# Kernel optimization log

Measured on AMD Instinct MI355X. Metric: run time of the kernel, lower is better.

## Reference

```python
import jax, jax.numpy as jnp
import numpy as np

EMBED_DIM = 768
NUM_HEADS = 12
HEAD_DIM = EMBED_DIM // NUM_HEADS // 2  # 32
MLP_DIM = 3072
DEPTH = 1
LAMBDA_INIT = 0.8 - 0.6 * float(np.exp(-0.3 * (DEPTH - 1)))  # 0.2
EPS = 1e-5


def layernorm(x, g, b):
    mu = jnp.mean(x, axis=-1, keepdims=True)
    var = jnp.mean((x - mu) ** 2, axis=-1, keepdims=True)
    return (x - mu) * jax.lax.rsqrt(var + EPS) * g + b


def rmsnorm(x, g):
    ms = jnp.mean(x ** 2, axis=-1, keepdims=True)
    return x * jax.lax.rsqrt(ms + EPS) * g


def setup_inputs() -> dict:
    key = jax.random.key(0)
    ks = jax.random.split(key, 16)
    d, m, hd = EMBED_DIM, MLP_DIM, HEAD_DIM
    inp = {
        "x": jax.random.normal(ks[0], (32, 577, d), dtype=jnp.float32),
        "ln1_g": jnp.ones((d,), jnp.float32),
        "ln1_b": jnp.zeros((d,), jnp.float32),
        "wq": jax.random.normal(ks[1], (d, d), jnp.float32) * 0.02,
        "wk": jax.random.normal(ks[2], (d, d), jnp.float32) * 0.02,
        "wv": jax.random.normal(ks[3], (d, d), jnp.float32) * 0.02,
        "wo": jax.random.normal(ks[4], (d, d), jnp.float32) * 0.02,
        "lq1": jax.random.normal(ks[5], (hd,), jnp.float32) * 0.1,
        "lk1": jax.random.normal(ks[6], (hd,), jnp.float32) * 0.1,
        "lq2": jax.random.normal(ks[7], (hd,), jnp.float32) * 0.1,
        "lk2": jax.random.normal(ks[8], (hd,), jnp.float32) * 0.1,
        "subln_g": jnp.ones((2 * hd,), jnp.float32),
        "ln2_g": jnp.ones((d,), jnp.float32),
        "ln2_b": jnp.zeros((d,), jnp.float32),
        "w1": jax.random.normal(ks[9], (m, d), jnp.float32) * 0.02,
        "b1": jnp.zeros((m,), jnp.float32),
        "w2": jax.random.normal(ks[10], (d, m), jnp.float32) * 0.02,
        "b2": jnp.zeros((d,), jnp.float32),
    }
    return inp


def diff_attn(x, wq, wk, wv, wo, lq1, lk1, lq2, lk2, subln_g):
    b, n, d = x.shape
    h, hd = NUM_HEADS, HEAD_DIM
    q = (x @ wq.T).reshape(b, n, 2 * h, hd)  # [b,n,2h,hd]
    k = (x @ wk.T).reshape(b, n, 2 * h, hd)
    v = (x @ wv.T).reshape(b, n, h, 2 * hd)  # [b,n,h,2hd]
    scale = hd ** -0.5
    scores = jnp.einsum("bnhd,bmhd->bhnm", q * scale, k)  # [b,2h,n,n]
    probs = jax.nn.softmax(scores.astype(jnp.float32), axis=-1).astype(x.dtype)
    probs = probs.reshape(b, h, 2, n, n)
    lam = jnp.exp(jnp.sum(lq1 * lk1)) - jnp.exp(jnp.sum(lq2 * lk2)) + LAMBDA_INIT
    attn = probs[:, :, 0] - lam * probs[:, :, 1]  # [b,h,n,n]
    out = jnp.einsum("bhnm,bmhe->bnhe", attn, v)  # [b,n,h,2hd]
    out = rmsnorm(out, subln_g) * (1.0 - LAMBDA_INIT)
    return out.reshape(b, n, d) @ wo.T


def reference(x, ln1_g, ln1_b, wq, wk, wv, wo, lq1, lk1, lq2, lk2, subln_g,
              ln2_g, ln2_b, w1, b1, w2, b2):
    # pre-LN -> differential attention -> residual
    a = diff_attn(layernorm(x, ln1_g, ln1_b), wq, wk, wv, wo,
                  lq1, lk1, lq2, lk2, subln_g)
    x = x + a
    # pre-LN -> GELU MLP -> residual (dropout = 0 / eval)
    h = layernorm(x, ln2_g, ln2_b)
    h = jax.nn.gelu(h @ w1.T + b1, approximate=False) @ w2.T + b2
    return x + h
```

## Files before the change

### kernel.cpp

```cpp
#include <hip/hip_runtime.h>
#include <hip/hip_bf16.h>
#include <cstdint>
#include <cstddef>

typedef __bf16 bf16_t;
typedef __attribute__((ext_vector_type(8))) __bf16 bf16x8;
typedef __attribute__((ext_vector_type(4))) __bf16 bf16x4;
typedef __attribute__((ext_vector_type(4))) float f32x4;
typedef __attribute__((ext_vector_type(4))) int int4v;
typedef __attribute__((ext_vector_type(2))) unsigned uintx2;

#define DEV static __device__ __forceinline__

#define BATCH 32
#define SEQ 577
#define DMODEL 768
#define MROWS (BATCH * SEQ)
#define MPAD 18688
#define NH 12
#define HDIM 32
#define EDIM 64
#define MLPD 3072
#define NPAD 640
#define QKVSTR 2304

DEV f32x4 mfma16(bf16x8 a, bf16x8 b, f32x4 c) {
    return __builtin_amdgcn_mfma_f32_16x16x32_bf16(a, b, c, 0, 0, 0);
}

DEV void gload16(const void* g, void* l) {
    __builtin_amdgcn_global_load_lds(
        (const __attribute__((address_space(1))) void*)(uintptr_t)g,
        (__attribute__((address_space(3))) void*)(uintptr_t)l,
        16, 0, 0);
}

DEV unsigned cvt_pk_bf16(float lo, float hi) {
    unsigned r;
    asm("v_cvt_pk_bf16_f32 %0, %1, %2" : "=v"(r) : "v"(lo), "v"(hi));
    return r;
}
DEV void plane16_swap(unsigned& a, unsigned& b) {
    asm("v_permlane16_swap_b32 %0, %1" : "+v"(a), "+v"(b));
}
DEV void plane32_swap(unsigned& a, unsigned& b) {
    asm("v_permlane32_swap_b32 %0, %1" : "+v"(a), "+v"(b));
}

DEV int xcd_swz(int orig, int nwg) {
    const int q = nwg >> 3, r = nwg & 7;
    const int xcd = orig & 7, loc = orig >> 3;
    return (xcd < r ? xcd * (q + 1) : r * (q + 1) + (xcd - r) * q) + loc;
}

__global__ __launch_bounds__(256)
void wconv_kernel(const float* __restrict__ wq, const float* __restrict__ wk,
                  const float* __restrict__ wv, const float* __restrict__ wo,
                  const float* __restrict__ w1, const float* __restrict__ w2,
                  bf16_t* __restrict__ dst)
{
    const size_t idx = ((size_t)blockIdx.x * 256 + threadIdx.x) * 4;
    const float* src;
    size_t off;
    if      (idx <  589824) { src = wq; off = idx; }
    else if (idx < 1179648) { src = wk; off = idx - 589824; }
    else if (idx < 1769472) { src = wv; off = idx - 1179648; }
    else if (idx < 2359296) { src = wo; off = idx - 1769472; }
    else if (idx < 4718592) { src = w1; off = idx - 2359296; }
    else                    { src = w2; off = idx - 4718592; }
    const f32x4 v = *(const f32x4*)&src[off];
    bf16x4 o;
#pragma unroll
    for (int u = 0; u < 4; ++u) o[u] = (bf16_t)v[u];
    *(bf16x4*)&dst[idx] = o;
}

__global__ void lam_kernel(const float* __restrict__ lq1, const float* __restrict__ lk1,
                           const float* __restrict__ lq2, const float* __restrict__ lk2,
                           float* __restrict__ lam)
{
    const int l = threadIdx.x;
    float a = 0.f, c = 0.f;
    if (l < 32) { a = lq1[l] * lk1[l]; c = lq2[l] * lk2[l]; }
#pragma unroll
    for (int m = 1; m < 32; m <<= 1) { a += __shfl_xor(a, m); c += __shfl_xor(c, m); }
    if (l == 0) *lam = expf(a) - expf(c) + 0.2f;
}

__global__ __launch_bounds__(256)
void ln_kernel(const float* __restrict__ src, const float* __restrict__ g,
               const float* __restrict__ bt, bf16_t* __restrict__ dst, const int Mv)
{
    const int row = blockIdx.x;
    const int t = threadIdx.x;
    if (row >= Mv) {
        for (int i = t; i < DMODEL; i += 256) dst[(size_t)row * DMODEL + i] = (bf16_t)0.f;
        return;
    }
    const float* p = src + (size_t)row * DMODEL;
    const float v0 = p[t], v1 = p[t + 256], v2 = p[t + 512];
    float s = v0 + v1 + v2, s2 = v0 * v0 + v1 * v1 + v2 * v2;
#pragma unroll
    for (int m = 1; m < 64; m <<= 1) { s += __shfl_xor(s, m); s2 += __shfl_xor(s2, m); }
    __shared__ float red[8];
    const int w = t >> 6;
    if ((t & 63) == 0) { red[w] = s; red[4 + w] = s2; }
    __syncthreads();
    s  = red[0] + red[1] + red[2] + red[3];
    s2 = red[4] + red[5] + red[6] + red[7];
    const float mu  = s * (1.f / DMODEL);
    const float var = s2 * (1.f / DMODEL) - mu * mu;
    const float rs = rsqrtf(var + 1e-5f);
    bf16_t* d = dst + (size_t)row * DMODEL;
    d[t      ] = (bf16_t)((v0 - mu) * rs * g[t      ] + bt[t      ]);
    d[t + 256] = (bf16_t)((v1 - mu) * rs * g[t + 256] + bt[t + 256]);
    d[t + 512] = (bf16_t)((v2 - mu) * rs * g[t + 512] + bt[t + 512]);
}

#define VM3 asm volatile("s_waitcnt vmcnt(3)" ::: "memory")
#define VM0 asm volatile("s_waitcnt vmcnt(0)" ::: "memory")
#define SB0 __builtin_amdgcn_sched_barrier(0)
#define BAR __builtin_amdgcn_s_barrier()

#define ASZ 4096
#define BSZ 8192

#define QUAD8(H, BP)                                                         \
    do {                                                                     \
        __builtin_amdgcn_s_setprio(1);                                       \
        _Pragma("unroll")                                                    \
        for (int m2_ = 0; m2_ < 4; ++m2_)                                    \
            _Pragma("unroll")                                                \
            for (int j_ = 0; j_ < 2; ++j_)                                   \
                acc[m2_][(H) * 2 + j_] =                                     \
                    mfma16(af[m2_], BP[j_], acc[m2_][(H) * 2 + j_]);         \
        __builtin_amdgcn_s_setprio(0);                                       \
    } while (0)

template <int EPI>
__global__ __launch_bounds__(512, 4)
void gemm4(const bf16_t* __restrict__ A, const bf16_t* __restrict__ W,
           const int K, const int N, const int NT,
           bf16_t* __restrict__ outB, float* __restrict__ outF,
           const float* __restrict__ bias, const float* __restrict__ resid,
           const int Mv)
{
    __shared__ bf16_t As[3 * ASZ];
    __shared__ bf16_t Bs[3 * BSZ];
    const int t = threadIdx.x;
    const int l = t & 63, w = t >> 6;
    const int lg = l >> 4, lc = l & 15;
    const int wr = w >> 2, wc = w & 3;

    const int nwg = gridDim.x * gridDim.y;
    const int orig = blockIdx.y * gridDim.x + blockIdx.x;
    const int wg = xcd_swz(orig, nwg);
    const int tileRow = (wg / gridDim.y) * 128;
    const int tileCol = (wg % gridDim.y) * 256;

    const int srow = t >> 2;
    const int csrc = ((t & 3) ^ ((t >> 3) & 3)) * 8;
    const bf16_t* srcA  = A + (size_t)(tileRow + srow) * K + csrc;
    const bf16_t* srcB0 = W + (size_t)(tileCol + srow) * K + csrc;
    const bf16_t* srcB1 = W + (size_t)(tileCol + 128 + srow) * K + csrc;

    f32x4 acc[4][4];
#pragma unroll
    for (int m = 0; m < 4; ++m)
#pragma unroll
        for (int n = 0; n < 4; ++n) acc[m][n] = f32x4{0.f, 0.f, 0.f, 0.f};

    const int rch = (lg ^ ((lc >> 1) & 3)) * 8;
    const int aoff = (wr * 64 + lc) * 32 + rch;
    const int boff = (wc * 64 + lc) * 32 + rch;

    bf16x8 af[4], b01[2], b23[2];

    auto stageA = [&](int kt, bf16_t* dst) {
        gload16(srcA + (size_t)kt * 32, dst + t * 8);
    };
    auto stageB = [&](int kt, bf16_t* dst) {
        gload16(srcB0 + (size_t)kt * 32, dst + t * 8);
        gload16(srcB1 + (size_t)kt * 32, dst + (t + 512) * 8);
    };
    auto rdA = [&](const bf16_t* buf) {
#pragma unroll
        for (int m2 = 0; m2 < 4; ++m2)
            af[m2] = *(const bf16x8*)&buf[aoff + m2 * 512];
    };
    auto rdB = [&](const bf16_t* buf, int h, bf16x8* bp) {
#pragma unroll
        for (int j = 0; j < 2; ++j)
            bp[j] = *(const bf16x8*)&buf[boff + (h * 2 + j) * 512];
    };

    auto STEP = [&](int kt, const bf16_t* AsR, const bf16_t* BsR,
                    bf16_t* AsS, bf16_t* BsS) {
        rdA(AsR); rdB(BsR, 0, b01);
        if (kt + 2 < NT) stageA(kt + 2, AsS);
        SB0; BAR; SB0;
        QUAD8(0, b01);
        BAR;
        rdB(BsR, 1, b23);
        if (kt + 2 < NT) stageB(kt + 2, BsS);
        if (kt == NT - 2) { VM0; } else if (kt < NT - 2) { VM3; }
        SB0; BAR; SB0;
        QUAD8(1, b23);
        BAR;
    };

    stageA(0, As);          stageB(0, Bs);
    stageA(1, As + ASZ);    stageB(1, Bs + BSZ);
    VM3; BAR;

#pragma unroll 1
    for (int kt = 0; kt < NT; kt += 3) {
        STEP(kt,     As,           Bs,           As + 2 * ASZ, Bs + 2 * BSZ);
        STEP(kt + 1, As + ASZ,     Bs + BSZ,     As,           Bs);
        STEP(kt + 2, As + 2 * ASZ, Bs + 2 * BSZ, As + ASZ,     Bs + BSZ);
    }

#pragma unroll
    for (int m = 0; m < 4; ++m) {
        const int row0 = tileRow + wr * 64 + m * 16 + 4 * lg;
#pragma unroll
        for (int n = 0; n < 4; ++n) {
            const int col = tileCol + wc * 64 + n * 16 + lc;
#pragma unroll
            for (int r = 0; r < 4; ++r) {
                const int row = row0 + r;
                float v = acc[m][n][r];
                if (EPI == 0) {
                    outB[(size_t)row * N + col] = (bf16_t)v;
                } else if (EPI == 1) {
                    const float xin = (row < Mv) ? resid[(size_t)row * N + col] : 0.f;
                    outF[(size_t)row * N + col] = v + xin;
                } else if (EPI == 2) {
                    v += bias[col];
                    v = 0.5f * v * (1.f + erff(v * 0.70710678118654752f));
                    outB[(size_t)row * N + col] = (bf16_t)v;
                } else {
                    if (row < Mv)
                        outF[(size_t)row * N + col] = v + bias[col] + resid[(size_t)row * N + col];
                }
            }
        }
    }
}

__global__ __launch_bounds__(256)
void vtrans_kernel(const bf16_t* __restrict__ qkv, bf16_t* __restrict__ vt)
{
    const int nt = blockIdx.x, h = blockIdx.y, b = blockIdx.z;
    const int t = threadIdx.x;
    __shared__ bf16_t T[64][72];
    {
        const int nl = t >> 2, e0 = (t & 3) * 16;
        const int n = nt * 64 + nl;
        bf16x8 a, c;
        if (n < SEQ) {
            const bf16_t* src = &qkv[((size_t)b * SEQ + n) * QKVSTR + 1536 + h * EDIM + e0];
            a = *(const bf16x8*)src;
            c = *(const bf16x8*)(src + 8);
        } else {
#pragma unroll
            for (int u = 0; u < 8; ++u) { a[u] = (bf16_t)0.f; c[u] = (bf16_t)0.f; }
        }
#pragma unroll
        for (int u = 0; u < 8; ++u) { T[e0 + u][nl] = a[u]; T[e0 + 8 + u][nl] = c[u]; }
    }
    __syncthreads();
    {
        const int e = t >> 2, n0 = (t & 3) * 16;
        bf16x8 a, c;
#pragma unroll
        for (int u = 0; u < 8; ++u) { a[u] = T[e][n0 + u]; c[u] = T[e][n0 + 8 + u]; }
        bf16_t* d = &vt[((size_t)(b * NH + h) * EDIM + e) * NPAD + nt * 64 + n0];
        *(bf16x8*)d = a;
        *(bf16x8*)(d + 8) = c;
    }
}

__global__ __launch_bounds__(256)
void attn_kernel(const bf16_t* __restrict__ qkv, const bf16_t* __restrict__ vtp,
                 const float* __restrict__ lamp, const float* __restrict__ subg,
                 bf16_t* __restrict__ outp)
{
    const int orig = blockIdx.x + 10 * (blockIdx.y + 12 * blockIdx.z);
    const int wg = xcd_swz(orig, 3840);
    const int qt = wg % 10;
    const int h  = (wg / 10) % 12;
    const int b  = wg / 120;
    const int t = threadIdx.x, w = t >> 6, l = t & 63;
    const int lg = l >> 4, lc = l & 15;
    const float lam = *lamp;
    const float SC2 = 0.25503487f;
    const float MARG = 8.0f * 0.25503487f;

    __shared__ bf16_t Ks[2][64 * 64];
    __shared__ bf16_t Vs[2][64 * 64];

    const size_t mb = (size_t)b * SEQ;
    const int q0row = qt * 64 + w * 16;

    bf16x8 qf[2];
#pragma unroll
    for (int hh = 0; hh < 2; ++hh)
        qf[hh] = *(const bf16x8*)&qkv[(mb + q0row + lc) * QKVSTR
                                      + h * 64 + hh * 32 + 8 * lg];

    f32x4 O[2][4];
    f32x4 Ol[2];
#pragma unroll
    for (int hh = 0; hh < 2; ++hh) {
        Ol[hh] = f32x4{0.f, 0.f, 0.f, 0.f};
#pragma unroll
        for (int ef = 0; ef < 4; ++ef) O[hh][ef] = f32x4{0.f, 0.f, 0.f, 0.f};
    }

    bf16x8 ones;
#pragma unroll
    for (int u = 0; u < 8; ++u) ones[u] = (bf16_t)1.0f;

    const int r0 = t >> 3, c0 = (t & 7);
    const int r1 = r0 + 32;
    const bf16_t* kg0 = &qkv[(mb + r0) * QKVSTR + 768 + h * 64 + ((c0 ^ (r0 & 7)) * 8)];
    const bf16_t* kg1 = &qkv[(mb + r1) * QKVSTR + 768 + h * 64 + ((c0 ^ (r1 & 7)) * 8)];
    const bf16_t* vg0 = &vtp[(size_t)((b * NH + h) * EDIM + r0) * NPAD + ((c0 ^ (r0 & 7)) * 8)];
    const bf16_t* vg1 = &vtp[(size_t)((b * NH + h) * EDIM + r1) * NPAD + ((c0 ^ (r1 & 7)) * 8)];

    auto stage = [&](int kt, int bufi) {
        gload16(kg0 + (size_t)kt * (64 * QKVSTR), &Ks[bufi][t * 8]);
        gload16(kg1 + (size_t)kt * (64 * QKVSTR), &Ks[bufi][(t + 256) * 8]);
        gload16(vg0 + kt * 64, &Vs[bufi][t * 8]);
        gload16(vg1 + kt * 64, &Vs[bufi][(t + 256) * 8]);
    };

    stage(0, 0);
    int buf = 0;

    const int swz = lc & 7;
    int koff[2], voff[2];
#pragma unroll
    for (int hh = 0; hh < 2; ++hh) koff[hh] = lc * 64 + (((hh * 4 + lg) ^ swz) * 8);
#pragma unroll
    for (int ks = 0; ks < 2; ++ks) voff[ks] = lc * 64 + (((ks * 4 + lg) ^ swz) * 8);

#pragma unroll 1
    for (int kt = 0; kt < 10; ++kt) {
        __builtin_amdgcn_s_barrier();
        if (kt < 9) {
            stage(kt + 1, buf ^ 1);
            asm volatile("s_waitcnt vmcnt(4)" ::: "memory");
        } else {
            VM0;
        }
        __builtin_amdgcn_s_barrier();
        __builtin_amdgcn_sched_barrier(0);

        const bf16_t* Kb = &Ks[buf][0];
        const bf16_t* Vb = &Vs[buf][0];

#pragma unroll
        for (int hh = 0; hh < 2; ++hh) {
            bf16x8 kf[4];
#pragma unroll
            for (int f = 0; f < 4; ++f)
                kf[f] = *(const bf16x8*)&Kb[koff[hh] + f * 1024];
            f32x4 s[4];
#pragma unroll
            for (int f = 0; f < 4; ++f)
                s[f] = mfma16(kf[f], qf[hh], f32x4{0.f, 0.f, 0.f, 0.f});
            if (kt == 9) {
#pragma unroll
                for (int f = 0; f < 4; ++f)
#pragma unroll
                    for (int r = 0; r < 4; ++r)
                        if (f | r) s[f][r] = -3e38f;
                if (lg != 0) s[0][0] = -3e38f;
            }
            unsigned wd[4][2];
#pragma unroll
            for (int f = 0; f < 4; ++f) {
                float p0 = __builtin_amdgcn_exp2f(__builtin_fmaf(s[f][0], SC2, -MARG));
                float p1 = __builtin_amdgcn_exp2f(__builtin_fmaf(s[f][1], SC2, -MARG));
                float p2 = __builtin_amdgcn_exp2f(__builtin_fmaf(s[f][2], SC2, -MARG));
                float p3 = __builtin_amdgcn_exp2f(__builtin_fmaf(s[f][3], SC2, -MARG));
                wd[f][0] = cvt_pk_bf16(p0, p1);
                wd[f][1] = cvt_pk_bf16(p2, p3);
            }
#pragma unroll
            for (int half = 0; half < 2; ++half) {
#pragma unroll
                for (int p = 0; p < 2; ++p) {
                    unsigned& Aa = wd[half * 2][p];
                    unsigned& Bb = wd[half * 2 + 1][p];
                    plane32_swap(Aa, Bb);
                    plane16_swap(Aa, Bb);
                }
            }
            const bf16x8 pa0 = __builtin_bit_cast(bf16x8,
                int4v{(int)wd[0][0], (int)wd[0][1], (int)wd[1][0], (int)wd[1][1]});
            const bf16x8 pa1 = __builtin_bit_cast(bf16x8,
                int4v{(int)wd[2][0], (int)wd[2][1], (int)wd[3][0], (int)wd[3][1]});

#pragma unroll
            for (int ef = 0; ef < 4; ++ef) {
                const bf16x8 vb0 = *(const bf16x8*)&Vb[voff[0] + ef * 1024];
                const bf16x8 vb1 = *(const bf16x8*)&Vb[voff[1] + ef * 1024];
                O[hh][ef] = mfma16(vb0, pa0, O[hh][ef]);
                O[hh][ef] = mfma16(vb1, pa1, O[hh][ef]);
            }
            Ol[hh] = mfma16(ones, pa0, Ol[hh]);
            Ol[hh] = mfma16(ones, pa1, Ol[hh]);
        }
        buf ^= 1;
    }

    {
        const float i0 = 1.f / Ol[0][0];
        const float i1 = lam / Ol[1][0];
        float comb[4][4];
        float ms = 0.f;
#pragma unroll
        for (int ef = 0; ef < 4; ++ef)
#pragma unroll
            for (int r = 0; r < 4; ++r) {
                const float o = O[0][ef][r] * i0 - O[1][ef][r] * i1;
                comb[ef][r] = o;
                ms += o * o;
            }
        ms += __shfl_xor(ms, 16);
        ms += __shfl_xor(ms, 32);
        const float sc = rsqrtf(ms * (1.f / 64.f) + 1e-5f) * 0.8f;
        const int nq = q0row + lc;
        if (nq < SEQ) {
            bf16_t* dst = &outp[(mb + nq) * DMODEL + h * EDIM + 4 * lg];
#pragma unroll
            for (int ef = 0; ef < 4; ++ef) {
                const f32x4 g4 = *(const f32x4*)&subg[ef * 16 + 4 * lg];
                const unsigned u0 = cvt_pk_bf16(comb[ef][0] * sc * g4[0],
                                                comb[ef][1] * sc * g4[1]);
                const unsigned u1 = cvt_pk_bf16(comb[ef][2] * sc * g4[2],
                                                comb[ef][3] * sc * g4[3]);
                *(uintx2*)(dst + ef * 16) = uintx2{u0, u1};
            }
        }
    }
}

extern "C" void kernel_launch(void* const* d_in, const int* in_sizes, int n_in,
                              void* d_out, int out_size, void* d_ws, size_t ws_size,
                              hipStream_t stream)
{
    const float* x    = (const float*)d_in[0];
    const float* ln1g = (const float*)d_in[1];
    const float* ln1b = (const float*)d_in[2];
    const float* wq   = (const float*)d_in[3];
    const float* wk   = (const float*)d_in[4];
    const float* wv   = (const float*)d_in[5];
    const float* wo   = (const float*)d_in[6];
    const float* lq1  = (const float*)d_in[7];
    const float* lk1  = (const float*)d_in[8];
    const float* lq2  = (const float*)d_in[9];
    const float* lk2  = (const float*)d_in[10];
    const float* subg = (const float*)d_in[11];
    const float* ln2g = (const float*)d_in[12];
    const float* ln2b = (const float*)d_in[13];
    const float* w1   = (const float*)d_in[14];
    const float* b1   = (const float*)d_in[15];
    const float* w2   = (const float*)d_in[16];
    const float* b2   = (const float*)d_in[17];

    char* ws = (char*)d_ws;
    bf16_t* wAll = (bf16_t*)ws;
    bf16_t* wob = wAll + 1769472;
    bf16_t* w1b = wAll + 2359296;
    bf16_t* w2b = wAll + 4718592;
    ws += 7077888ull * 2;
    float* lamP = (float*)ws; ws += 256;
    bf16_t* xn   = (bf16_t*)ws; ws += (size_t)MPAD * DMODEL * 2;
    bf16_t* qkvb = (bf16_t*)ws;
    bf16_t* h1   = qkvb;
    ws += (size_t)MPAD * QKVSTR * 2;
    bf16_t* vtb  = (bf16_t*)ws; ws += (size_t)(BATCH * NH) * EDIM * NPAD * 2;
    bf16_t* aout = (bf16_t*)ws; ws += (size_t)MPAD * DMODEL * 2;
    float* x1    = (float*)ws;  ws += (size_t)MPAD * DMODEL * 4;

    wconv_kernel<<<6912, 256, 0, stream>>>(wq, wk, wv, wo, w1, w2, wAll);
    lam_kernel<<<1, 64, 0, stream>>>(lq1, lk1, lq2, lk2, lamP);
    ln_kernel<<<MPAD, 256, 0, stream>>>(x, ln1g, ln1b, xn, MROWS);

    gemm4<0><<<dim3(146, 9), 512, 0, stream>>>(xn, wAll, 768, QKVSTR, 24,
                                               qkvb, nullptr, nullptr, nullptr, MROWS);

    vtrans_kernel<<<dim3(10, 12, 32), 256, 0, stream>>>(qkvb, vtb);
    attn_kernel<<<dim3(10, 12, 32), 256, 0, stream>>>(qkvb, vtb, lamP, subg, aout);

    gemm4<1><<<dim3(146, 3), 512, 0, stream>>>(aout, wob, 768, 768, 24,
                                               nullptr, x1, nullptr, x, MROWS);
    ln_kernel<<<MPAD, 256, 0, stream>>>(x1, ln2g, ln2b, xn, MROWS);
    gemm4<2><<<dim3(146, 12), 512, 0, stream>>>(xn, w1b, 768, MLPD, 24,
                                                h1, nullptr, b1, nullptr, MROWS);
    gemm4<3><<<dim3(146, 3), 512, 0, stream>>>(h1, w2b, MLPD, 768, 96,
                                               nullptr, (float*)d_out, b2, x1, MROWS);
}
```

Before: 559.1 us.

## Split attention differential halves across separate waves with 512-thread blocks

The attention kernel now launches 512 threads. Each pair of waves handles one 16-row query slice, with one wave per differential half (hh), instead of a single wave looping over both halves. The second-half wave writes its O accumulators and row sums to shared memory reused from the K/V buffers, and the first-half wave combines them after a barrier. This doubles the waves available to hide latency and halves per-wave register pressure, at the cost of an extra LDS round trip and barrier in the epilogue.

```diff
diff --git a/kernel.cpp b/kernel.cpp
--- a/kernel.cpp
+++ b/kernel.cpp
@@ -118,6 +118,7 @@
 }
 
 #define VM3 asm volatile("s_waitcnt vmcnt(3)" ::: "memory")
+#define VM2 asm volatile("s_waitcnt vmcnt(2)" ::: "memory")
 #define VM0 asm volatile("s_waitcnt vmcnt(0)" ::: "memory")
 #define SB0 __builtin_amdgcn_sched_barrier(0)
 #define BAR __builtin_amdgcn_s_barrier()
@@ -281,7 +282,7 @@
     }
 }
 
-__global__ __launch_bounds__(256)
+__global__ __launch_bounds__(512)
 void attn_kernel(const bf16_t* __restrict__ qkv, const bf16_t* __restrict__ vtp,
                  const float* __restrict__ lamp, const float* __restrict__ subg,
                  bf16_t* __restrict__ outp)
@@ -293,6 +294,7 @@
     const int b  = wg / 120;
     const int t = threadIdx.x, w = t >> 6, l = t & 63;
     const int lg = l >> 4, lc = l & 15;
+    const int qsub = w >> 1, hh = w & 1;
     const float lam = *lamp;
     const float SC2 = 0.25503487f;
     const float MARG = 8.0f * 0.25503487f;
@@ -301,132 +303,133 @@
     __shared__ bf16_t Vs[2][64 * 64];
 
     const size_t mb = (size_t)b * SEQ;
-    const int q0row = qt * 64 + w * 16;
-
-    bf16x8 qf[2];
-#pragma unroll
-    for (int hh = 0; hh < 2; ++hh)
-        qf[hh] = *(const bf16x8*)&qkv[(mb + q0row + lc) * QKVSTR
-                                      + h * 64 + hh * 32 + 8 * lg];
-
-    f32x4 O[2][4];
-    f32x4 Ol[2];
-#pragma unroll
-    for (int hh = 0; hh < 2; ++hh) {
-        Ol[hh] = f32x4{0.f, 0.f, 0.f, 0.f};
-#pragma unroll
-        for (int ef = 0; ef < 4; ++ef) O[hh][ef] = f32x4{0.f, 0.f, 0.f, 0.f};
-    }
+    const int q0row = qt * 64 + qsub * 16;
+
+    const bf16x8 qf = *(const bf16x8*)&qkv[(mb + q0row + lc) * QKVSTR
+                                           + h * 64 + hh * 32 + 8 * lg];
+
+    f32x4 O[4];
+    f32x4 Ol = f32x4{0.f, 0.f, 0.f, 0.f};
+#pragma unroll
+    for (int ef = 0; ef < 4; ++ef) O[ef] = f32x4{0.f, 0.f, 0.f, 0.f};
 
     bf16x8 ones;
 #pragma unroll
     for (int u = 0; u < 8; ++u) ones[u] = (bf16_t)1.0f;
 
-    const int r0 = t >> 3, c0 = (t & 7);
-    const int r1 = r0 + 32;
-    const bf16_t* kg0 = &qkv[(mb + r0) * QKVSTR + 768 + h * 64 + ((c0 ^ (r0 & 7)) * 8)];
-    const bf16_t* kg1 = &qkv[(mb + r1) * QKVSTR + 768 + h * 64 + ((c0 ^ (r1 & 7)) * 8)];
-    const bf16_t* vg0 = &vtp[(size_t)((b * NH + h) * EDIM + r0) * NPAD + ((c0 ^ (r0 & 7)) * 8)];
-    const bf16_t* vg1 = &vtp[(size_t)((b * NH + h) * EDIM + r1) * NPAD + ((c0 ^ (r1 & 7)) * 8)];
+    const int r0 = t >> 3, c0 = t & 7;
+    const bf16_t* kg = &qkv[(mb + r0) * QKVSTR + 768 + h * 64 + ((c0 ^ (r0 & 7)) * 8)];
+    const bf16_t* vg = &vtp[(size_t)((b * NH + h) * EDIM + r0) * NPAD + ((c0 ^ (r0 & 7)) * 8)];
 
     auto stage = [&](int kt, int bufi) {
-        gload16(kg0 + (size_t)kt * (64 * QKVSTR), &Ks[bufi][t * 8]);
-        gload16(kg1 + (size_t)kt * (64 * QKVSTR), &Ks[bufi][(t + 256) * 8]);
-        gload16(vg0 + kt * 64, &Vs[bufi][t * 8]);
-        gload16(vg1 + kt * 64, &Vs[bufi][(t + 256) * 8]);
+        gload16(kg + (size_t)kt * (64 * QKVSTR), &Ks[bufi][t * 8]);
+        gload16(vg + kt * 64, &Vs[bufi][t * 8]);
     };
 
     stage(0, 0);
     int buf = 0;
 
     const int swz = lc & 7;
-    int koff[2], voff[2];
-#pragma unroll
-    for (int hh = 0; hh < 2; ++hh) koff[hh] = lc * 64 + (((hh * 4 + lg) ^ swz) * 8);
+    const int koff = lc * 64 + (((hh * 4 + lg) ^ swz) * 8);
+    int voff[2];
 #pragma unroll
     for (int ks = 0; ks < 2; ++ks) voff[ks] = lc * 64 + (((ks * 4 + lg) ^ swz) * 8);
 
 #pragma unroll 1
     for (int kt = 0; kt < 10; ++kt) {
-        __builtin_amdgcn_s_barrier();
+        BAR;
         if (kt < 9) {
             stage(kt + 1, buf ^ 1);
-            asm volatile("s_waitcnt vmcnt(4)" ::: "memory");
+            VM2;
         } else {
             VM0;
         }
-        __builtin_amdgcn_s_barrier();
-        __builtin_amdgcn_sched_barrier(0);
+        BAR;
+        SB0;
 
         const bf16_t* Kb = &Ks[buf][0];
         const bf16_t* Vb = &Vs[buf][0];
 
-#pragma unroll
-        for (int hh = 0; hh < 2; ++hh) {
-            bf16x8 kf[4];
+        bf16x8 kf[4];
+#pragma unroll
+        for (int f = 0; f < 4; ++f)
+            kf[f] = *(const bf16x8*)&Kb[koff + f * 1024];
+        f32x4 s[4];
+#pragma unroll
+        for (int f = 0; f < 4; ++f)
+            s[f] = mfma16(kf[f], qf, f32x4{0.f, 0.f, 0.f, 0.f});
+        if (kt == 9) {
 #pragma unroll
             for (int f = 0; f < 4; ++f)
-                kf[f] = *(const bf16x8*)&Kb[koff[hh] + f * 1024];
-            f32x4 s[4];
-#pragma unroll
-            for (int f = 0; f < 4; ++f)
-                s[f] = mfma16(kf[f], qf[hh], f32x4{0.f, 0.f, 0.f, 0.f});
-            if (kt == 9) {
-#pragma unroll
-                for (int f = 0; f < 4; ++f)
-#pragma unroll
-                    for (int r = 0; r < 4; ++r)
-                        if (f | r) s[f][r] = -3e38f;
-                if (lg != 0) s[0][0] = -3e38f;
+#pragma unroll
+                for (int r = 0; r < 4; ++r)
+                    if (f | r) s[f][r] = -3e38f;
+            if (lg != 0) s[0][0] = -3e38f;
+        }
+        unsigned wd[4][2];
+#pragma unroll
+        for (int f = 0; f < 4; ++f) {
+            float p0 = __builtin_amdgcn_exp2f(__builtin_fmaf(s[f][0], SC2, -MARG));
+            float p1 = __builtin_amdgcn_exp2f(__builtin_fmaf(s[f][1], SC2, -MARG));
+            float p2 = __builtin_amdgcn_exp2f(__builtin_fmaf(s[f][2], SC2, -MARG));
+            float p3 = __builtin_amdgcn_exp2f(__builtin_fmaf(s[f][3], SC2, -MARG));
+            wd[f][0] = cvt_pk_bf16(p0, p1);
+            wd[f][1] = cvt_pk_bf16(p2, p3);
+        }
+#pragma unroll
+        for (int half = 0; half < 2; ++half) {
+#pragma unroll
+            for (int p = 0; p < 2; ++p) {
+                unsigned& Aa = wd[half * 2][p];
+                unsigned& Bb = wd[half * 2 + 1][p];
+                plane32_swap(Aa, Bb);
+                plane16_swap(Aa, Bb);
             }
-            unsigned wd[4][2];
-#pragma unroll
-            for (int f = 0; f < 4; ++f) {
-                float p0 = __builtin_amdgcn_exp2f(__builtin_fmaf(s[f][0], SC2, -MARG));
-                float p1 = __builtin_amdgcn_exp2f(__builtin_fmaf(s[f][1], SC2, -MARG));
-                float p2 = __builtin_amdgcn_exp2f(__builtin_fmaf(s[f][2], SC2, -MARG));
-                float p3 = __builtin_amdgcn_exp2f(__builtin_fmaf(s[f][3], SC2, -MARG));
-                wd[f][0] = cvt_pk_bf16(p0, p1);
-                wd[f][1] = cvt_pk_bf16(p2, p3);
-            }
-#pragma unroll
-            for (int half = 0; half < 2; ++half) {
-#pragma unroll
-                for (int p = 0; p < 2; ++p) {
-                    unsigned& Aa = wd[half * 2][p];
-                    unsigned& Bb = wd[half * 2 + 1][p];
-                    plane32_swap(Aa, Bb);
-                    plane16_swap(Aa, Bb);
-                }
-            }
-            const bf16x8 pa0 = __builtin_bit_cast(bf16x8,
-                int4v{(int)wd[0][0], (int)wd[0][1], (int)wd[1][0], (int)wd[1][1]});
-            const bf16x8 pa1 = __builtin_bit_cast(bf16x8,
-                int4v{(int)wd[2][0], (int)wd[2][1], (int)wd[3][0], (int)wd[3][1]});
-
-#pragma unroll
-            for (int ef = 0; ef < 4; ++ef) {
-                const bf16x8 vb0 = *(const bf16x8*)&Vb[voff[0] + ef * 1024];
-                const bf16x8 vb1 = *(const bf16x8*)&Vb[voff[1] + ef * 1024];
-                O[hh][ef] = mfma16(vb0, pa0, O[hh][ef]);
-                O[hh][ef] = mfma16(vb1, pa1, O[hh][ef]);
-            }
-            Ol[hh] = mfma16(ones, pa0, Ol[hh]);
-            Ol[hh] = mfma16(ones, pa1, Ol[hh]);
-        }
+        }
+        const bf16x8 pa0 = __builtin_bit_cast(bf16x8,
+            int4v{(int)wd[0][0], (int)wd[0][1], (int)wd[1][0], (int)wd[1][1]});
+        const bf16x8 pa1 = __builtin_bit_cast(bf16x8,
+            int4v{(int)wd[2][0], (int)wd[2][1], (int)wd[3][0], (int)wd[3][1]});
+
+#pragma unroll
+        for (int ef = 0; ef < 4; ++ef) {
+            const bf16x8 vb0 = *(const bf16x8*)&Vb[voff[0] + ef * 1024];
+            const bf16x8 vb1 = *(const bf16x8*)&Vb[voff[1] + ef * 1024];
+            O[ef] = mfma16(vb0, pa0, O[ef]);
+            O[ef] = mfma16(vb1, pa1, O[ef]);
+        }
+        Ol = mfma16(ones, pa0, Ol);
+        Ol = mfma16(ones, pa1, Ol);
         buf ^= 1;
     }
 
-    {
-        const float i0 = 1.f / Ol[0][0];
-        const float i1 = lam / Ol[1][0];
+    float* oscr = (float*)&Ks[0][0];
+    float* lscr = (float*)&Vs[0][0];
+
+    BAR;
+    if (hh == 1) {
+        float* od = oscr + qsub * 1024;
+#pragma unroll
+        for (int ef = 0; ef < 4; ++ef)
+#pragma unroll
+            for (int r = 0; r < 4; ++r)
+                od[(ef * 16 + 4 * lg + r) * 16 + lc] = O[ef][r];
+        lscr[qsub * 16 + lc] = Ol[0];
+    }
+    asm volatile("s_waitcnt lgkmcnt(0)" ::: "memory");
+    BAR;
+    if (hh == 0) {
+        const float i0 = 1.f / Ol[0];
+        const float i1 = lam / lscr[qsub * 16 + lc];
+        const float* od = oscr + qsub * 1024;
         float comb[4][4];
         float ms = 0.f;
 #pragma unroll
         for (int ef = 0; ef < 4; ++ef)
 #pragma unroll
             for (int r = 0; r < 4; ++r) {
-                const float o = O[0][ef][r] * i0 - O[1][ef][r] * i1;
+                const float o = O[ef][r] * i0
+                              - od[(ef * 16 + 4 * lg + r) * 16 + lc] * i1;
                 comb[ef][r] = o;
                 ms += o * o;
             }
@@ -495,7 +498,7 @@
                                                qkvb, nullptr, nullptr, nullptr, MROWS);
 
     vtrans_kernel<<<dim3(10, 12, 32), 256, 0, stream>>>(qkvb, vtb);
-    attn_kernel<<<dim3(10, 12, 32), 256, 0, stream>>>(qkvb, vtb, lamP, subg, aout);
+    attn_kernel<<<dim3(10, 12, 32), 512, 0, stream>>>(qkvb, vtb, lamP, subg, aout);
 
     gemm4<1><<<dim3(146, 3), 512, 0, stream>>>(aout, wob, 768, 768, 24,
                                                nullptr, x1, nullptr, x, MROWS);
```

Result: faster. 541.8 us (-3.1%).
